# Kernel tuning notes

Hardware: AMD Instinct MI355X
Metric: run time of the kernel (lower is better)

The kernel has to match this reference:

```python
import jax, jax.numpy as jnp
import numpy as np

TEMPERATURE = 0.2
IOU_THRES = 0.4
PER_IMG = 256  # proposals per image, hard-coded in the original forward
EPS = 1e-12    # F.normalize eps


def setup_inputs() -> dict:
    key = jax.random.key(0)
    k1, k2, k3 = jax.random.split(key, 3)
    B, D, K = 128, 1024, 4
    N = B * PER_IMG
    box_cls_feat_con = jax.random.normal(k1, (N, D), dtype=jnp.float32)
    crop_feat_con = jax.random.normal(k2, (K, B, D), dtype=jnp.float32)
    ious = jax.random.uniform(k3, (N,), dtype=jnp.float32)
    return {
        "box_cls_feat_con": box_cls_feat_con,
        "crop_feat_con": crop_feat_con,
        "batch_size": B,
        "ious": ious,
    }


def _l2_normalize(x):
    return x / jnp.clip(jnp.linalg.norm(x, axis=-1, keepdims=True), EPS)


def reference(box_cls_feat_con, crop_feat_con, batch_size, ious):
    B = batch_size
    N, D = box_cls_feat_con.shape
    P = PER_IMG
    # [B, P, D] normalized box features
    box_n = _l2_normalize(box_cls_feat_con.reshape(B, P, D))
    # crop features are detached (z = crop_feat.detach())
    z_n = _l2_normalize(jax.lax.stop_gradient(crop_feat_con))  # [K, B, D]
    # cosine similarity of each proposal with its image's crop feature, per scale
    cos = jnp.einsum("bpd,kbd->kbp", box_n, z_n)  # [K, B, P]
    pos_mask = (ious >= IOU_THRES).reshape(B, P)  # [B, P]
    cnt_pos = pos_mask.sum(-1).astype(cos.dtype)  # [B]
    cnt_neg = (P - cnt_pos)
    # Cos_Distance = -mean(cosine_sim) over the masked group
    sim_pos = -(cos * pos_mask).sum(-1) / cnt_pos          # [K, B]
    sim_neg = -(cos * (~pos_mask)).sum(-1) / cnt_neg       # [K, B]
    # -log(exp(sp/T) / (exp(sp/T) + exp(sn/T))) = softplus((sn - sp)/T)
    L = jax.nn.softplus((sim_neg - sim_pos) / TEMPERATURE).sum(-1)  # [K]
    return jnp.min(L) / B
```

## Files before the change

### kernel.cpp

```cpp
#include <hip/hip_runtime.h>
#include <cstdint>
#include <cstddef>

#define PD 1024
#define PER_IMG 256
#define TEMP_INV 5.0f
#define IOU_THRES 0.4f
#define SPLIT 8
#define RPB (PER_IMG / SPLIT)
#define RW  (RPB / 4)

typedef float f32x4 __attribute__((ext_vector_type(4)));

__device__ inline f32x4 ntload4(const float* p) {
    return __builtin_nontemporal_load(reinterpret_cast<const f32x4*>(p));
}

__global__ __launch_bounds__(256) void k1_rowsum(
    const float* __restrict__ box, const float* __restrict__ ious,
    const float* __restrict__ crop,
    float* __restrict__ wsP, float* __restrict__ wsA,
    float* __restrict__ wsZ, float* __restrict__ wsCnt, int B, int K)
{
    const int b    = blockIdx.x / SPLIT;
    const int s    = blockIdx.x % SPLIT;
    const int lane = threadIdx.x & 63;
    const int wv   = threadIdx.x >> 6;
    const int row0 = s * RPB + wv * RW;

    float accP[16], accA[16];
#pragma unroll
    for (int i = 0; i < 16; ++i) { accP[i] = 0.f; accA[i] = 0.f; }
    int cnt = 0;

    const size_t growBase = (size_t)b * PER_IMG + row0;
    const float* rp = box + growBase * PD;

#pragma unroll 1
    for (int it = 0; it < RW; it += 4) {
        f32x4 v[4][4];
#pragma unroll
        for (int r = 0; r < 4; ++r)
#pragma unroll
            for (int j = 0; j < 4; ++j)
                v[r][j] = ntload4(rp + (size_t)(it + r) * PD + (j * 64 + lane) * 4);

        float iou[4];
#pragma unroll
        for (int r = 0; r < 4; ++r) iou[r] = ious[growBase + it + r];

        float ss[4];
#pragma unroll
        for (int r = 0; r < 4; ++r) {
            float t = 0.f;
#pragma unroll
            for (int j = 0; j < 4; ++j)
                t += v[r][j][0] * v[r][j][0] + v[r][j][1] * v[r][j][1]
                   + v[r][j][2] * v[r][j][2] + v[r][j][3] * v[r][j][3];
            ss[r] = t;
        }
#pragma unroll
        for (int off = 32; off >= 1; off >>= 1) {
#pragma unroll
            for (int r = 0; r < 4; ++r)
                ss[r] += __shfl_xor(ss[r], off, 64);
        }

#pragma unroll
        for (int r = 0; r < 4; ++r) {
            const float inv = 1.0f / fmaxf(sqrtf(ss[r]), 1e-12f);
            const bool pos = iou[r] >= IOU_THRES;
            if (pos && lane == 0) ++cnt;
            const float pm = pos ? inv : 0.f;
#pragma unroll
            for (int j = 0; j < 4; ++j) {
#pragma unroll
                for (int c = 0; c < 4; ++c) {
                    accA[j * 4 + c] += v[r][j][c] * inv;
                    accP[j * 4 + c] += v[r][j][c] * pm;
                }
            }
        }
    }

    __shared__ float ldsP[4][PD];
    __shared__ float ldsA[4][PD];
    __shared__ int cntLds;
    if (threadIdx.x == 0) cntLds = 0;
#pragma unroll
    for (int j = 0; j < 4; ++j) {
        const int d = (j * 64 + lane) * 4;
        f32x4 p = { accP[j*4+0], accP[j*4+1], accP[j*4+2], accP[j*4+3] };
        f32x4 a = { accA[j*4+0], accA[j*4+1], accA[j*4+2], accA[j*4+3] };
        *reinterpret_cast<f32x4*>(&ldsP[wv][d]) = p;
        *reinterpret_cast<f32x4*>(&ldsA[wv][d]) = a;
    }
    __syncthreads();
    if (lane == 0 && cnt) atomicAdd(&cntLds, cnt);

    if (wv < K) {
        const float* zp = crop + ((size_t)wv * B + b) * PD;
        float dotP = 0.f, dotA = 0.f, ssz = 0.f;
#pragma unroll
        for (int j = 0; j < 4; ++j) {
            const int d = (j * 64 + lane) * 4;
            const f32x4 z  = *reinterpret_cast<const f32x4*>(zp + d);
            f32x4 sP = *reinterpret_cast<const f32x4*>(&ldsP[0][d]);
            f32x4 sA = *reinterpret_cast<const f32x4*>(&ldsA[0][d]);
#pragma unroll
            for (int w = 1; w < 4; ++w) {
                sP += *reinterpret_cast<const f32x4*>(&ldsP[w][d]);
                sA += *reinterpret_cast<const f32x4*>(&ldsA[w][d]);
            }
#pragma unroll
            for (int c = 0; c < 4; ++c) {
                dotP += sP[c] * z[c];
                dotA += sA[c] * z[c];
                ssz  += z[c]  * z[c];
            }
        }
#pragma unroll
        for (int off = 32; off >= 1; off >>= 1) {
            dotP += __shfl_xor(dotP, off, 64);
            dotA += __shfl_xor(dotA, off, 64);
            ssz  += __shfl_xor(ssz,  off, 64);
        }
        if (lane == 0) {
            const size_t kb = (size_t)wv * B + b;
            wsP[kb * SPLIT + s] = dotP;
            wsA[kb * SPLIT + s] = dotA;
            if (s == 0) wsZ[kb] = ssz;
        }
    }
    __syncthreads();
    if (threadIdx.x == 0) wsCnt[b * SPLIT + s] = (float)cntLds;
}

__global__ __launch_bounds__(256) void k2_final(
    const float* __restrict__ wsP, const float* __restrict__ wsA,
    const float* __restrict__ wsZ, const float* __restrict__ wsCnt,
    float* __restrict__ out, int B, int K)
{
    const int t    = threadIdx.x;
    const int lane = t & 63;
    const int wv   = t >> 6;

    __shared__ float spl[512];
    __shared__ float red[4];

    for (int pair = t; pair < K * B; pair += 256) {
        const int b = pair % B;
        float P = 0.f, A = 0.f, C = 0.f;
#pragma unroll
        for (int s = 0; s < SPLIT; ++s) {
            P += wsP[(size_t)pair * SPLIT + s];
            A += wsA[(size_t)pair * SPLIT + s];
            C += wsCnt[b * SPLIT + s];
        }
        const float invz = 1.0f / fmaxf(sqrtf(wsZ[pair]), 1e-12f);
        const float simP = -(P * invz) / C;
        const float simN = -((A - P) * invz) / ((float)PER_IMG - C);
        const float x = (simN - simP) * TEMP_INV;
        spl[pair] = fmaxf(x, 0.f) + log1pf(expf(-fabsf(x)));
    }
    __syncthreads();

    if (wv < K) {
        float v = 0.f;
        for (int b = lane; b < B; b += 64) v += spl[wv * B + b];
#pragma unroll
        for (int off = 32; off >= 1; off >>= 1)
            v += __shfl_xor(v, off, 64);
        if (lane == 0) red[wv] = v;
    }
    __syncthreads();
    if (t == 0) {
        float m = red[0];
        for (int k = 1; k < K; ++k) m = fminf(m, red[k]);
        out[0] = m / (float)B;
    }
}

extern "C" void kernel_launch(void* const* d_in, const int* in_sizes, int n_in,
                              void* d_out, int out_size, void* d_ws, size_t ws_size,
                              hipStream_t stream)
{
    const float* box  = (const float*)d_in[0];
    const float* crop = (const float*)d_in[1];
    const float* ious = (const float*)d_in[3];

    const int N = in_sizes[3];
    const int B = N / PER_IMG;
    const int D = in_sizes[0] / N;
    const int K = in_sizes[1] / (B * D);

    char* w = (char*)d_ws;
    float* wsP   = (float*)w;  w += (size_t)K * B * SPLIT * sizeof(float);
    float* wsA   = (float*)w;  w += (size_t)K * B * SPLIT * sizeof(float);
    float* wsZ   = (float*)w;  w += (size_t)K * B * sizeof(float);
    float* wsCnt = (float*)w;

    hipLaunchKernelGGL(k1_rowsum, dim3(B * SPLIT), dim3(256), 0, stream,
                       box, ious, crop, wsP, wsA, wsZ, wsCnt, B, K);
    hipLaunchKernelGGL(k2_final, dim3(1), dim3(256), 0, stream,
                       wsP, wsA, wsZ, wsCnt, (float*)d_out, B, K);
}
```

Baseline: 31.44 us.

## Fuse final reduction into main kernel via last-block atomic counter

Merges the two kernels into one: each block bumps a global atomic counter after writing its partials, and the last block to arrive runs the final softplus/min reduction. The per-block cross-wave reduction no longer goes through 32KB of LDS staging of P/A vectors; each wave instead dots its own accumulators with all K crop vectors and reduces the scalars. This aims to remove a kernel launch gap and cut LDS usage, which can help occupancy. In exchange it adds a memset launch, redundant crop loads per wave, and hard-codes K=4 and a power-of-two B.

```diff
diff --git a/kernel.cpp b/kernel.cpp
--- a/kernel.cpp
+++ b/kernel.cpp
@@ -9,6 +9,7 @@
 #define SPLIT 8
 #define RPB (PER_IMG / SPLIT)
 #define RW  (RPB / 4)
+#define K4  4
 
 typedef float f32x4 __attribute__((ext_vector_type(4)));
 
@@ -16,17 +17,28 @@
     return __builtin_nontemporal_load(reinterpret_cast<const f32x4*>(p));
 }
 
-__global__ __launch_bounds__(256) void k1_rowsum(
+__global__ __launch_bounds__(256) void k1_fused(
     const float* __restrict__ box, const float* __restrict__ ious,
     const float* __restrict__ crop,
     float* __restrict__ wsP, float* __restrict__ wsA,
-    float* __restrict__ wsZ, float* __restrict__ wsCnt, int B, int K)
+    float* __restrict__ wsZ, float* __restrict__ wsCnt,
+    unsigned int* __restrict__ counter,
+    float* __restrict__ out, int B, int K)
 {
     const int b    = blockIdx.x / SPLIT;
     const int s    = blockIdx.x % SPLIT;
-    const int lane = threadIdx.x & 63;
-    const int wv   = threadIdx.x >> 6;
+    const int t    = threadIdx.x;
+    const int lane = t & 63;
+    const int wv   = t >> 6;
     const int row0 = s * RPB + wv * RW;
+    const int nblk = B * SPLIT;
+
+    __shared__ float ldsD[4][2 * K4];
+    __shared__ float ldsZ[K4];
+    __shared__ int   cntLds;
+    __shared__ int   lastFlag;
+    __shared__ float spl[512];
+    __shared__ float red[K4];
 
     float accP[16], accA[16];
 #pragma unroll
@@ -52,12 +64,12 @@
         float ss[4];
 #pragma unroll
         for (int r = 0; r < 4; ++r) {
-            float t = 0.f;
+            float acc = 0.f;
 #pragma unroll
             for (int j = 0; j < 4; ++j)
-                t += v[r][j][0] * v[r][j][0] + v[r][j][1] * v[r][j][1]
-                   + v[r][j][2] * v[r][j][2] + v[r][j][3] * v[r][j][3];
-            ss[r] = t;
+                acc += v[r][j][0] * v[r][j][0] + v[r][j][1] * v[r][j][1]
+                     + v[r][j][2] * v[r][j][2] + v[r][j][3] * v[r][j][3];
+            ss[r] = acc;
         }
 #pragma unroll
         for (int off = 32; off >= 1; off >>= 1) {
@@ -83,79 +95,79 @@
         }
     }
 
-    __shared__ float ldsP[4][PD];
-    __shared__ float ldsA[4][PD];
-    __shared__ int cntLds;
-    if (threadIdx.x == 0) cntLds = 0;
-#pragma unroll
-    for (int j = 0; j < 4; ++j) {
-        const int d = (j * 64 + lane) * 4;
-        f32x4 p = { accP[j*4+0], accP[j*4+1], accP[j*4+2], accP[j*4+3] };
-        f32x4 a = { accA[j*4+0], accA[j*4+1], accA[j*4+2], accA[j*4+3] };
-        *reinterpret_cast<f32x4*>(&ldsP[wv][d]) = p;
-        *reinterpret_cast<f32x4*>(&ldsA[wv][d]) = a;
-    }
+    if (t == 0) { cntLds = 0; lastFlag = 0; }
     __syncthreads();
     if (lane == 0 && cnt) atomicAdd(&cntLds, cnt);
 
-    if (wv < K) {
-        const float* zp = crop + ((size_t)wv * B + b) * PD;
-        float dotP = 0.f, dotA = 0.f, ssz = 0.f;
+    float dP[K4], dA[K4], zz[K4];
+#pragma unroll
+    for (int k = 0; k < K4; ++k) {
+        const float* zp = crop + ((size_t)k * B + b) * PD;
+        float p = 0.f, a = 0.f, z2 = 0.f;
 #pragma unroll
         for (int j = 0; j < 4; ++j) {
             const int d = (j * 64 + lane) * 4;
-            const f32x4 z  = *reinterpret_cast<const f32x4*>(zp + d);
-            f32x4 sP = *reinterpret_cast<const f32x4*>(&ldsP[0][d]);
-            f32x4 sA = *reinterpret_cast<const f32x4*>(&ldsA[0][d]);
-#pragma unroll
-            for (int w = 1; w < 4; ++w) {
-                sP += *reinterpret_cast<const f32x4*>(&ldsP[w][d]);
-                sA += *reinterpret_cast<const f32x4*>(&ldsA[w][d]);
+            const f32x4 z = *reinterpret_cast<const f32x4*>(zp + d);
+#pragma unroll
+            for (int c = 0; c < 4; ++c) {
+                p  += accP[j * 4 + c] * z[c];
+                a  += accA[j * 4 + c] * z[c];
+                z2 += z[c] * z[c];
             }
-#pragma unroll
-            for (int c = 0; c < 4; ++c) {
-                dotP += sP[c] * z[c];
-                dotA += sA[c] * z[c];
-                ssz  += z[c]  * z[c];
-            }
-        }
-#pragma unroll
-        for (int off = 32; off >= 1; off >>= 1) {
-            dotP += __shfl_xor(dotP, off, 64);
-            dotA += __shfl_xor(dotA, off, 64);
-            ssz  += __shfl_xor(ssz,  off, 64);
-        }
-        if (lane == 0) {
-            const size_t kb = (size_t)wv * B + b;
-            wsP[kb * SPLIT + s] = dotP;
-            wsA[kb * SPLIT + s] = dotA;
-            if (s == 0) wsZ[kb] = ssz;
-        }
-    }
-    __syncthreads();
-    if (threadIdx.x == 0) wsCnt[b * SPLIT + s] = (float)cntLds;
-}
-
-__global__ __launch_bounds__(256) void k2_final(
-    const float* __restrict__ wsP, const float* __restrict__ wsA,
-    const float* __restrict__ wsZ, const float* __restrict__ wsCnt,
-    float* __restrict__ out, int B, int K)
-{
-    const int t    = threadIdx.x;
-    const int lane = t & 63;
-    const int wv   = t >> 6;
-
-    __shared__ float spl[512];
-    __shared__ float red[4];
-
-    for (int pair = t; pair < K * B; pair += 256) {
-        const int b = pair % B;
+        }
+        dP[k] = p; dA[k] = a; zz[k] = z2;
+    }
+#pragma unroll
+    for (int off = 32; off >= 1; off >>= 1) {
+#pragma unroll
+        for (int k = 0; k < K4; ++k) {
+            dP[k] += __shfl_xor(dP[k], off, 64);
+            dA[k] += __shfl_xor(dA[k], off, 64);
+            zz[k] += __shfl_xor(zz[k], off, 64);
+        }
+    }
+    if (lane == 0) {
+#pragma unroll
+        for (int k = 0; k < K4; ++k) {
+            ldsD[wv][k]      = dP[k];
+            ldsD[wv][K4 + k] = dA[k];
+        }
+        if (wv == 0)
+#pragma unroll
+            for (int k = 0; k < K4; ++k) ldsZ[k] = zz[k];
+    }
+    __syncthreads();
+
+    if (t < 2 * K4) {
+        const float v = ldsD[0][t] + ldsD[1][t] + ldsD[2][t] + ldsD[3][t];
+        const int k = (t < K4) ? t : (t - K4);
+        const size_t kb = (size_t)k * B + b;
+        if (t < K4) wsP[kb * SPLIT + s] = v;
+        else        wsA[kb * SPLIT + s] = v;
+    }
+    if (s == 0 && t >= 8 && t < 8 + K4) wsZ[(size_t)(t - 8) * B + b] = ldsZ[t - 8];
+    if (t == 12) wsCnt[b * SPLIT + s] = (float)cntLds;
+    __syncthreads();
+
+    if (t == 0) {
+        __threadfence();
+        const unsigned old = atomicAdd(counter, 1u);
+        if (old == (unsigned)(nblk - 1)) lastFlag = 1;
+    }
+    __syncthreads();
+    if (!lastFlag) return;
+
+    __threadfence();
+
+    const int KB = K4 * B;
+    for (int pair = t; pair < KB; pair += 256) {
+        const int bb = pair & (B - 1);
         float P = 0.f, A = 0.f, C = 0.f;
 #pragma unroll
-        for (int s = 0; s < SPLIT; ++s) {
-            P += wsP[(size_t)pair * SPLIT + s];
-            A += wsA[(size_t)pair * SPLIT + s];
-            C += wsCnt[b * SPLIT + s];
+        for (int sp = 0; sp < SPLIT; ++sp) {
+            P += wsP[(size_t)pair * SPLIT + sp];
+            A += wsA[(size_t)pair * SPLIT + sp];
+            C += wsCnt[bb * SPLIT + sp];
         }
         const float invz = 1.0f / fmaxf(sqrtf(wsZ[pair]), 1e-12f);
         const float simP = -(P * invz) / C;
@@ -165,9 +177,9 @@
     }
     __syncthreads();
 
-    if (wv < K) {
+    if (wv < K4) {
         float v = 0.f;
-        for (int b = lane; b < B; b += 64) v += spl[wv * B + b];
+        for (int bb = lane; bb < B; bb += 64) v += spl[wv * B + bb];
 #pragma unroll
         for (int off = 32; off >= 1; off >>= 1)
             v += __shfl_xor(v, off, 64);
@@ -176,7 +188,7 @@
     __syncthreads();
     if (t == 0) {
         float m = red[0];
-        for (int k = 1; k < K; ++k) m = fminf(m, red[k]);
+        for (int k = 1; k < K4; ++k) m = fminf(m, red[k]);
         out[0] = m / (float)B;
     }
 }
@@ -195,13 +207,14 @@
     const int K = in_sizes[1] / (B * D);
 
     char* w = (char*)d_ws;
-    float* wsP   = (float*)w;  w += (size_t)K * B * SPLIT * sizeof(float);
-    float* wsA   = (float*)w;  w += (size_t)K * B * SPLIT * sizeof(float);
-    float* wsZ   = (float*)w;  w += (size_t)K * B * sizeof(float);
-    float* wsCnt = (float*)w;
-
-    hipLaunchKernelGGL(k1_rowsum, dim3(B * SPLIT), dim3(256), 0, stream,
-                       box, ious, crop, wsP, wsA, wsZ, wsCnt, B, K);
-    hipLaunchKernelGGL(k2_final, dim3(1), dim3(256), 0, stream,
-                       wsP, wsA, wsZ, wsCnt, (float*)d_out, B, K);
+    float* wsP   = (float*)w;  w += (size_t)K4 * B * SPLIT * sizeof(float);
+    float* wsA   = (float*)w;  w += (size_t)K4 * B * SPLIT * sizeof(float);
+    float* wsZ   = (float*)w;  w += (size_t)K4 * B * sizeof(float);
+    float* wsCnt = (float*)w;  w += (size_t)B * SPLIT * sizeof(float);
+    unsigned int* counter = (unsigned int*)w;
+
+    hipMemsetAsync(counter, 0, sizeof(unsigned int), stream);
+    hipLaunchKernelGGL(k1_fused, dim3(B * SPLIT), dim3(256), 0, stream,
+                       box, ious, crop, wsP, wsA, wsZ, wsCnt, counter,
+                       (float*)d_out, B, K);
 }
```

Result: slower. 61.16 us (+94.5%).
